# Performance work log

Hardware: AMD Instinct MI355X
Metric: run time of the kernel (lower is better)

## Reference

```python
import jax, jax.numpy as jnp
import numpy as np

B, D, C = 32, 30, 4        # batch, input spatial, in-channels
KS = 3                     # kernel size per dim
OD = D - KS + 1            # 28 (valid padding, stride 1)
P = OD ** 3                # 21952 output positions
K = (KS ** 3) * C          # 108 taps per output position
F = 4                      # output filters


def _patches(x):
    # x: [B, D, D, D, C] -> [B, P, K]
    xt = jnp.transpose(x, (0, 4, 1, 2, 3))  # NCDHW
    p = jax.lax.conv_general_dilated_patches(
        xt, filter_shape=(KS, KS, KS), window_strides=(1, 1, 1), padding='VALID')
    # p: [B, C*KS^3, OD, OD, OD]
    p = jnp.transpose(p, (0, 2, 3, 4, 1))
    return p.reshape(p.shape[0], P, K)


def _local_conv(x, W):
    # Locally-connected 3D conv (unshared weights) == structured sparse matmul.
    # W: [P, K, F] one weight per (output position, tap, filter).
    return jnp.einsum('bpk,pkf->bpf', _patches(x), W)


def setup_inputs() -> dict:
    key = jax.random.key(0)
    ks = jax.random.split(key, 7)
    x = jax.random.normal(ks[0], (B, D, D, D, C), jnp.float32)
    kernel_loc = jax.random.normal(ks[1], (P, K, F), jnp.float32) * 0.05
    kernel_rho = jax.random.normal(ks[2], (P, K, F), jnp.float32) * 0.1 - 5.0  # softplus -> small scale
    bias = jax.random.normal(ks[3], (F,), jnp.float32) * 0.05
    eps = jax.random.normal(ks[4], (P, K, F), jnp.float32)
    sign_in = jax.random.rademacher(ks[5], (B, D, D, D, C), jnp.float32)
    sign_out = jax.random.rademacher(ks[6], (B, P, F), jnp.float32)
    return dict(x=x, kernel_loc=kernel_loc, kernel_rho=kernel_rho, bias=bias,
                eps=eps, sign_in=sign_in, sign_out=sign_out)


def reference(x, kernel_loc, kernel_rho, bias, eps, sign_in, sign_out):
    # Flipout estimator: deterministic mean path + sign-perturbed noise path.
    scale = jax.nn.softplus(kernel_rho)
    out = _local_conv(x, kernel_loc)                                  # [B, P, F]
    out = out + sign_out * _local_conv(x * sign_in, scale * eps)      # flipout perturbation
    out = out + bias                                                  # per-filter bias (channels_last)
    return out.reshape(x.shape[0], OD, OD, OD, F)
```

## Files before the change

kernel.cpp:

```cpp
#include <hip/hip_runtime.h>


constexpr int Bn   = 32;
constexpr int Dn   = 30;
constexpr int Cn   = 4;
constexpr int ODn  = 28;
constexpr int Pn   = ODn * ODn * ODn;
constexpr int Tt   = 27;
constexpr int Kn   = Tt * Cn;
constexpr int PPB  = 16;
constexpr int NT   = Pn / PPB;
constexpr int THREADS = 512;
constexpr int WSTRIDE = Kn + 1;
constexpr int GRID = NT;

__device__ __forceinline__ unsigned bf16rne(float f) {
    unsigned u = __float_as_uint(f);
    return (u + 0x7fffu + ((u >> 16) & 1u)) >> 16;
}
__device__ __forceinline__ float bflo(unsigned u) { return __uint_as_float(u << 16); }
__device__ __forceinline__ float bfhi(unsigned u) { return __uint_as_float(u & 0xffff0000u); }

__device__ __forceinline__ uint4 pack_w(const float4 L, const float4 R, const float4 E) {
    float nx = (R.x > 15.f ? R.x : __logf(1.f + __expf(R.x))) * E.x;
    float ny = (R.y > 15.f ? R.y : __logf(1.f + __expf(R.y))) * E.y;
    float nz = (R.z > 15.f ? R.z : __logf(1.f + __expf(R.z))) * E.z;
    float nw = (R.w > 15.f ? R.w : __logf(1.f + __expf(R.w))) * E.w;
    uint4 pk;
    pk.x = bf16rne(L.x) | (bf16rne(L.y) << 16);
    pk.y = bf16rne(L.z) | (bf16rne(L.w) << 16);
    pk.z = bf16rne(nx)  | (bf16rne(ny) << 16);
    pk.w = bf16rne(nz)  | (bf16rne(nw) << 16);
    return pk;
}

__global__ __launch_bounds__(THREADS) void lc3d_flipout_kernel(
    const float* __restrict__ x,
    const float* __restrict__ loc,
    const float* __restrict__ rho,
    const float* __restrict__ bias,
    const float* __restrict__ eps,
    const float* __restrict__ sgn_in,
    const float* __restrict__ sgn_out,
    float* __restrict__ out)
{
    __shared__ uint4 wsh[PPB * WSTRIDE];

    const int tid = threadIdx.x;

    const int xcd  = blockIdx.x & 7;
    const int slot = blockIdx.x >> 3;
    const int Tx = (xcd < 4) ? xcd * 172 : 688 + (xcd - 4) * 171;
    const int p_base = (Tx + slot) * PPB;

    {
        const float4* loc4 = (const float4*)loc + (size_t)p_base * Kn;
        const float4* rho4 = (const float4*)rho + (size_t)p_base * Kn;
        const float4* eps4 = (const float4*)eps + (size_t)p_base * Kn;
        const int g0 = tid, g1 = tid + 512, g2 = tid + 1024;
        const float4 L0 = loc4[g0], R0 = rho4[g0], E0 = eps4[g0];
        const float4 L1 = loc4[g1], R1 = rho4[g1], E1 = eps4[g1];
        const float4 L2 = loc4[g2], R2 = rho4[g2], E2 = eps4[g2];
        {
            const int plc = g0 / Kn, k = g0 - plc * Kn;
            wsh[plc * WSTRIDE + k] = pack_w(L0, R0, E0);
        }
        {
            const int plc = g1 / Kn, k = g1 - plc * Kn;
            wsh[plc * WSTRIDE + k] = pack_w(L1, R1, E1);
        }
        {
            const int plc = g2 / Kn, k = g2 - plc * Kn;
            wsh[plc * WSTRIDE + k] = pack_w(L2, R2, E2);
        }
        if (tid < PPB * Kn - 1536) {
            const int g3 = tid + 1536;
            const int plc = g3 / Kn, k = g3 - plc * Kn;
            wsh[plc * WSTRIDE + k] = pack_w(loc4[g3], rho4[g3], eps4[g3]);
        }
    }
    __syncthreads();

    const int pl = tid & 15;
    const int b  = tid >> 4;
    const int p  = p_base + pl;
    const int od = p / (ODn * ODn);
    const int prem = p - od * (ODn * ODn);
    const int oh = prem / ODn;
    const int ow = prem - oh * ODn;
    const float4* x4 = (const float4*)x;
    const float4* s4 = (const float4*)sgn_in;
    const size_t v0 = (((size_t)b * Dn + od) * Dn + oh) * Dn + ow;
    const uint4* wp = wsh + pl * WSTRIDE;

    float a0=0.f,a1=0.f,a2=0.f,a3=0.f, n0=0.f,n1=0.f,n2=0.f,n3=0.f;

#define CHAN(c, x_c, s_c)                                                    \
    {                                                                        \
        const uint4 wv = wp[(c) * Tt + t];                                   \
        const float m0 = bflo(wv.x), m1 = bfhi(wv.x);                        \
        const float m2 = bflo(wv.y), m3 = bfhi(wv.y);                        \
        const float q0 = bflo(wv.z), q1 = bfhi(wv.z);                        \
        const float q2 = bflo(wv.w), q3 = bfhi(wv.w);                        \
        a0 = fmaf(x_c, m0, a0); a1 = fmaf(x_c, m1, a1);                      \
        a2 = fmaf(x_c, m2, a2); a3 = fmaf(x_c, m3, a3);                      \
        const float ya = (x_c) * (s_c);                                      \
        n0 = fmaf(ya, q0, n0); n1 = fmaf(ya, q1, n1);                        \
        n2 = fmaf(ya, q2, n2); n3 = fmaf(ya, q3, n3);                        \
    }

    #pragma unroll
    for (int kd = 0; kd < 3; ++kd) {
        #pragma unroll
        for (int kh = 0; kh < 3; ++kh) {
            const int roff = (kd * Dn + kh) * Dn;
            #pragma unroll
            for (int kw = 0; kw < 3; ++kw) {
                const int t = (kd * 3 + kh) * 3 + kw;
                const float4 xa = x4[v0 + roff + kw];
                const float4 sa = s4[v0 + roff + kw];
                CHAN(0, xa.x, sa.x);
                CHAN(1, xa.y, sa.y);
                CHAN(2, xa.z, sa.z);
                CHAN(3, xa.w, sa.w);
            }
        }
    }
#undef CHAN

    const float4 bi = *(const float4*)bias;
    const size_t ob = (size_t)b * Pn + p;
    const float4 so = ((const float4*)sgn_out)[ob];
    float4 o;
    o.x = fmaf(so.x, n0, a0) + bi.x;
    o.y = fmaf(so.y, n1, a1) + bi.y;
    o.z = fmaf(so.z, n2, a2) + bi.z;
    o.w = fmaf(so.w, n3, a3) + bi.w;
    ((float4*)out)[ob] = o;
}

extern "C" void kernel_launch(void* const* d_in, const int* in_sizes, int n_in,
                              void* d_out, int out_size, void* d_ws, size_t ws_size,
                              hipStream_t stream) {
    const float* x    = (const float*)d_in[0];
    const float* loc  = (const float*)d_in[1];
    const float* rho  = (const float*)d_in[2];
    const float* bias = (const float*)d_in[3];
    const float* eps  = (const float*)d_in[4];
    const float* si   = (const float*)d_in[5];
    const float* so   = (const float*)d_in[6];
    float* out = (float*)d_out;

    lc3d_flipout_kernel<<<dim3(GRID), dim3(THREADS), 0, stream>>>(
        x, loc, rho, bias, eps, si, so, out);
}
```

Before: 206.1 us.

## Make kernel persistent with double-buffered weight prefetch interleaved with compute

```diff
diff --git a/kernel.cpp b/kernel.cpp
--- a/kernel.cpp
+++ b/kernel.cpp
@@ -8,11 +8,14 @@
 constexpr int Pn   = ODn * ODn * ODn;
 constexpr int Tt   = 27;
 constexpr int Kn   = Tt * Cn;
-constexpr int PPB  = 16;
+constexpr int PPB  = 8;
 constexpr int NT   = Pn / PPB;
-constexpr int THREADS = 512;
+constexpr int THREADS = 256;
 constexpr int WSTRIDE = Kn + 1;
-constexpr int GRID = NT;
+constexpr int UNITS = PPB * Kn;
+constexpr int TPX  = NT / 8;
+constexpr int SLOTS = 128;
+constexpr int GRID = SLOTS * 8;
 
 __device__ __forceinline__ unsigned bf16rne(float f) {
     unsigned u = __float_as_uint(f);
@@ -44,56 +47,46 @@
     const float* __restrict__ sgn_out,
     float* __restrict__ out)
 {
-    __shared__ uint4 wsh[PPB * WSTRIDE];
+    __shared__ uint4 wsh[2][PPB * WSTRIDE];
 
     const int tid = threadIdx.x;
 
     const int xcd  = blockIdx.x & 7;
     const int slot = blockIdx.x >> 3;
-    const int Tx = (xcd < 4) ? xcd * 172 : 688 + (xcd - 4) * 171;
-    const int p_base = (Tx + slot) * PPB;
+    const int tA = (slot * TPX) >> 7;
+    const int tB = ((slot + 1) * TPX) >> 7;
+    const int T0 = xcd * TPX + tA;
+    const int n  = tB - tA;
+
+    const float4* loc4 = (const float4*)loc;
+    const float4* rho4 = (const float4*)rho;
+    const float4* eps4 = (const float4*)eps;
+    const float4* x4   = (const float4*)x;
+    const float4* s4   = (const float4*)sgn_in;
+    const float4  bi   = *(const float4*)bias;
+
+    const int pl = tid & 7;
+    const int b  = tid >> 3;
+    const bool tail = (tid < UNITS - 3 * THREADS);
+
+    const int g0 = tid, g1 = tid + 256, g2 = tid + 512, g3 = tid + 768;
+    const int o0 = (g0 / Kn) * WSTRIDE + (g0 % Kn);
+    const int o1 = (g1 / Kn) * WSTRIDE + (g1 % Kn);
+    const int o2 = (g2 / Kn) * WSTRIDE + (g2 % Kn);
+    const int o3 = (g3 / Kn) * WSTRIDE + (g3 % Kn);
 
     {
-        const float4* loc4 = (const float4*)loc + (size_t)p_base * Kn;
-        const float4* rho4 = (const float4*)rho + (size_t)p_base * Kn;
-        const float4* eps4 = (const float4*)eps + (size_t)p_base * Kn;
-        const int g0 = tid, g1 = tid + 512, g2 = tid + 1024;
-        const float4 L0 = loc4[g0], R0 = rho4[g0], E0 = eps4[g0];
-        const float4 L1 = loc4[g1], R1 = rho4[g1], E1 = eps4[g1];
-        const float4 L2 = loc4[g2], R2 = rho4[g2], E2 = eps4[g2];
-        {
-            const int plc = g0 / Kn, k = g0 - plc * Kn;
-            wsh[plc * WSTRIDE + k] = pack_w(L0, R0, E0);
-        }
-        {
-            const int plc = g1 / Kn, k = g1 - plc * Kn;
-            wsh[plc * WSTRIDE + k] = pack_w(L1, R1, E1);
-        }
-        {
-            const int plc = g2 / Kn, k = g2 - plc * Kn;
-            wsh[plc * WSTRIDE + k] = pack_w(L2, R2, E2);
-        }
-        if (tid < PPB * Kn - 1536) {
-            const int g3 = tid + 1536;
-            const int plc = g3 / Kn, k = g3 - plc * Kn;
-            wsh[plc * WSTRIDE + k] = pack_w(loc4[g3], rho4[g3], eps4[g3]);
-        }
+        const size_t base = (size_t)T0 * UNITS;
+        const float4 L0 = loc4[base + g0], R0 = rho4[base + g0], E0 = eps4[base + g0];
+        const float4 L1 = loc4[base + g1], R1 = rho4[base + g1], E1 = eps4[base + g1];
+        const float4 L2 = loc4[base + g2], R2 = rho4[base + g2], E2 = eps4[base + g2];
+        wsh[0][o0] = pack_w(L0, R0, E0);
+        wsh[0][o1] = pack_w(L1, R1, E1);
+        wsh[0][o2] = pack_w(L2, R2, E2);
+        if (tail)
+            wsh[0][o3] = pack_w(loc4[base + g3], rho4[base + g3], eps4[base + g3]);
     }
     __syncthreads();
-
-    const int pl = tid & 15;
-    const int b  = tid >> 4;
-    const int p  = p_base + pl;
-    const int od = p / (ODn * ODn);
-    const int prem = p - od * (ODn * ODn);
-    const int oh = prem / ODn;
-    const int ow = prem - oh * ODn;
-    const float4* x4 = (const float4*)x;
-    const float4* s4 = (const float4*)sgn_in;
-    const size_t v0 = (((size_t)b * Dn + od) * Dn + oh) * Dn + ow;
-    const uint4* wp = wsh + pl * WSTRIDE;
-
-    float a0=0.f,a1=0.f,a2=0.f,a3=0.f, n0=0.f,n1=0.f,n2=0.f,n3=0.f;
 
 #define CHAN(c, x_c, s_c)                                                    \
     {                                                                        \
@@ -109,34 +102,73 @@
         n2 = fmaf(ya, q2, n2); n3 = fmaf(ya, q3, n3);                        \
     }
 
-    #pragma unroll
-    for (int kd = 0; kd < 3; ++kd) {
-        #pragma unroll
-        for (int kh = 0; kh < 3; ++kh) {
-            const int roff = (kd * Dn + kh) * Dn;
-            #pragma unroll
-            for (int kw = 0; kw < 3; ++kw) {
-                const int t = (kd * 3 + kh) * 3 + kw;
-                const float4 xa = x4[v0 + roff + kw];
-                const float4 sa = s4[v0 + roff + kw];
-                CHAN(0, xa.x, sa.x);
-                CHAN(1, xa.y, sa.y);
-                CHAN(2, xa.z, sa.z);
-                CHAN(3, xa.w, sa.w);
-            }
+#define CHUNK(t_lo, t_hi)                                                    \
+    _Pragma("unroll")                                                        \
+    for (int t = (t_lo); t < (t_hi); ++t) {                                  \
+        const int kd = t / 9, kh = (t % 9) / 3, kw = t % 3;                  \
+        const int off = (kd * Dn + kh) * Dn + kw;                            \
+        const float4 xa = x4[v0 + off];                                      \
+        const float4 sa = s4[v0 + off];                                      \
+        CHAN(0, xa.x, sa.x);                                                 \
+        CHAN(1, xa.y, sa.y);                                                 \
+        CHAN(2, xa.z, sa.z);                                                 \
+        CHAN(3, xa.w, sa.w);                                                 \
+    }
+
+#pragma unroll 1
+    for (int i = 0; i < n; ++i) {
+        const int cur = i & 1;
+        const int T = T0 + i;
+        const int p = T * PPB + pl;
+        const int od = p / (ODn * ODn);
+        const int prem = p - od * (ODn * ODn);
+        const int oh = prem / ODn;
+        const int ow = prem - oh * ODn;
+        const size_t v0 = (((size_t)b * Dn + od) * Dn + oh) * Dn + ow;
+        const uint4* wp = &wsh[cur][pl * WSTRIDE];
+        const bool pf = (i + 1 < n);
+        const size_t nb = (size_t)(T + 1) * UNITS;
+
+        float a0=0.f,a1=0.f,a2=0.f,a3=0.f, n0=0.f,n1=0.f,n2=0.f,n3=0.f;
+
+        float4 PL0, PR0, PE0, PL1, PR1, PE1, PL2, PR2, PE2, PL3, PR3, PE3;
+        if (pf) { PL0 = loc4[nb + g0]; PR0 = rho4[nb + g0]; PE0 = eps4[nb + g0]; }
+
+        CHUNK(0, 9)
+
+        if (pf) {
+            wsh[cur ^ 1][o0] = pack_w(PL0, PR0, PE0);
+            PL1 = loc4[nb + g1]; PR1 = rho4[nb + g1]; PE1 = eps4[nb + g1];
+            if (tail) { PL3 = loc4[nb + g3]; PR3 = rho4[nb + g3]; PE3 = eps4[nb + g3]; }
         }
+
+        CHUNK(9, 18)
+
+        if (pf) {
+            wsh[cur ^ 1][o1] = pack_w(PL1, PR1, PE1);
+            PL2 = loc4[nb + g2]; PR2 = rho4[nb + g2]; PE2 = eps4[nb + g2];
+        }
+
+        CHUNK(18, 27)
+
+        if (pf) {
+            wsh[cur ^ 1][o2] = pack_w(PL2, PR2, PE2);
+            if (tail) wsh[cur ^ 1][o3] = pack_w(PL3, PR3, PE3);
+        }
+
+        const size_t ob = (size_t)b * Pn + p;
+        const float4 so = ((const float4*)sgn_out)[ob];
+        float4 o;
+        o.x = fmaf(so.x, n0, a0) + bi.x;
+        o.y = fmaf(so.y, n1, a1) + bi.y;
+        o.z = fmaf(so.z, n2, a2) + bi.z;
+        o.w = fmaf(so.w, n3, a3) + bi.w;
+        ((float4*)out)[ob] = o;
+
+        __syncthreads();
     }
+#undef CHUNK
 #undef CHAN
-
-    const float4 bi = *(const float4*)bias;
-    const size_t ob = (size_t)b * Pn + p;
-    const float4 so = ((const float4*)sgn_out)[ob];
-    float4 o;
-    o.x = fmaf(so.x, n0, a0) + bi.x;
-    o.y = fmaf(so.y, n1, a1) + bi.y;
-    o.z = fmaf(so.z, n2, a2) + bi.z;
-    o.w = fmaf(so.w, n3, a3) + bi.w;
-    ((float4*)out)[ob] = o;
 }
 
 extern "C" void kernel_launch(void* const* d_in, const int* in_sizes, int n_in,
```

After: 534.8 us. 159% more time.

## Prepack noise weights to bf16 workspace and stream tiles via async LDS double-buffering

Applied to the files above, without the earlier changes.

```diff
diff --git a/kernel.cpp b/kernel.cpp
--- a/kernel.cpp
+++ b/kernel.cpp
@@ -8,11 +8,22 @@
 constexpr int Pn   = ODn * ODn * ODn;
 constexpr int Tt   = 27;
 constexpr int Kn   = Tt * Cn;
-constexpr int PPB  = 16;
+constexpr int PPB  = 8;
 constexpr int NT   = Pn / PPB;
-constexpr int THREADS = 512;
-constexpr int WSTRIDE = Kn + 1;
-constexpr int GRID = NT;
+constexpr int TPX  = NT / 8;
+
+constexpr int THREADS_B = 256;
+constexpr int SLOTS  = 96;
+constexpr int GRID_B = SLOTS * 8;
+constexpr int LOC_UNITS   = PPB * Kn;
+constexpr int NOISE_UNITS = PPB * Kn / 2;
+constexpr int TILE_UNITS  = LOC_UNITS + NOISE_UNITS;
+constexpr int NCHUNK = 21;
+constexpr int BUF_UNITS = NCHUNK * 64;
+constexpr int NOISE_BYTES_PER_TILE = PPB * Kn * 8;
+constexpr int LOC_BYTES_PER_TILE   = PPB * Kn * 16;
+
+constexpr size_t WS_NEEDED = (size_t)Pn * Kn * 8;
 
 __device__ __forceinline__ unsigned bf16rne(float f) {
     unsigned u = __float_as_uint(f);
@@ -20,6 +31,175 @@
 }
 __device__ __forceinline__ float bflo(unsigned u) { return __uint_as_float(u << 16); }
 __device__ __forceinline__ float bfhi(unsigned u) { return __uint_as_float(u & 0xffff0000u); }
+
+typedef const __attribute__((address_space(1))) void GASV;
+typedef __attribute__((address_space(3))) void LASV;
+__device__ __forceinline__ void gld_lds16(const void* g, void* l) {
+    __builtin_amdgcn_global_load_lds((GASV*)g, (LASV*)l, 16, 0, 0);
+}
+
+__global__ __launch_bounds__(256) void pack_noise_kernel(
+    const float* __restrict__ rho, const float* __restrict__ eps,
+    uint2* __restrict__ ws)
+{
+    const long NU = (long)Pn * Kn;
+    const float4* r4 = (const float4*)rho;
+    const float4* e4 = (const float4*)eps;
+    for (long g = (long)blockIdx.x * 256 + threadIdx.x; g < NU;
+         g += (long)gridDim.x * 256) {
+        const float4 R = r4[g];
+        const float4 E = e4[g];
+        const float nx = (R.x > 15.f ? R.x : __logf(1.f + __expf(R.x))) * E.x;
+        const float ny = (R.y > 15.f ? R.y : __logf(1.f + __expf(R.y))) * E.y;
+        const float nz = (R.z > 15.f ? R.z : __logf(1.f + __expf(R.z))) * E.z;
+        const float nw = (R.w > 15.f ? R.w : __logf(1.f + __expf(R.w))) * E.w;
+        uint2 o;
+        o.x = bf16rne(nx) | (bf16rne(ny) << 16);
+        o.y = bf16rne(nz) | (bf16rne(nw) << 16);
+        ws[g] = o;
+    }
+}
+
+__global__ __launch_bounds__(THREADS_B) void lc3d_flipout_dma(
+    const float* __restrict__ x,
+    const float* __restrict__ loc,
+    const float* __restrict__ bias,
+    const uint2* __restrict__ ws,
+    const float* __restrict__ sgn_in,
+    const float* __restrict__ sgn_out,
+    float* __restrict__ out)
+{
+    __shared__ uint4 wsh[2][BUF_UNITS];
+
+    const int tid = threadIdx.x;
+    const int wv = tid >> 6, ln = tid & 63;
+
+    const int xcd  = blockIdx.x & 7;
+    const int slot = blockIdx.x >> 3;
+    const int tA = (slot * TPX) / SLOTS;
+    const int tB = ((slot + 1) * TPX) / SLOTS;
+    const int T0 = xcd * TPX + tA;
+    const int n  = tB - tA;
+
+    const int nch = (wv == 0) ? 6 : 5;
+    const int cb  = (wv == 0) ? 0 : (1 + 5 * wv);
+    int  coff[6];
+    bool cws[6];
+    int  cchk[6];
+    #pragma unroll
+    for (int j = 0; j < 6; ++j) {
+        int ch = (j < nch) ? (cb + j) : cb;
+        const int u = ch * 64 + ln;
+        if (u < LOC_UNITS) {
+            const int k = u >> 3, pp = u & 7;
+            coff[j] = pp * (Kn * 16) + k * 16;
+            cws[j] = false;
+        } else if (u < TILE_UNITS) {
+            coff[j] = (u - LOC_UNITS) * 16;
+            cws[j] = true;
+        } else {
+            coff[j] = 0; cws[j] = false;
+        }
+        cchk[j] = ch;
+    }
+
+#define ISSUE(TT, BI)                                                        \
+    {                                                                        \
+        const char* bl = (const char*)loc + (size_t)(TT) * LOC_BYTES_PER_TILE;   \
+        const char* bw = (const char*)ws  + (size_t)(TT) * NOISE_BYTES_PER_TILE; \
+        char* lb = (char*)&wsh[BI][0];                                       \
+        _Pragma("unroll")                                                    \
+        for (int j = 0; j < 6; ++j)                                          \
+            if (j < nch)                                                     \
+                gld_lds16((cws[j] ? bw : bl) + coff[j], lb + cchk[j] * 1024); \
+    }
+
+    ISSUE(T0, 0)
+    asm volatile("s_waitcnt vmcnt(0)" ::: "memory");
+    __syncthreads();
+
+    const float4* x4 = (const float4*)x;
+    const float4* s4 = (const float4*)sgn_in;
+    const float4  bi = *(const float4*)bias;
+    const int pl = tid & 7;
+    const int b  = tid >> 3;
+
+    float4 o_prev;
+    size_t ob_prev = 0;
+    bool have_prev = false;
+
+#define CHAN(c, x_c, s_c)                                                    \
+    {                                                                        \
+        const int kk = (c) * Tt + t;                                         \
+        const float4 m = *(const float4*)&lc4[kk * 8 + pl];                  \
+        const uint2 nz = nz2[pl * Kn + kk];                                  \
+        a0 = fmaf(x_c, m.x, a0); a1 = fmaf(x_c, m.y, a1);                    \
+        a2 = fmaf(x_c, m.z, a2); a3 = fmaf(x_c, m.w, a3);                    \
+        const float ya = (x_c) * (s_c);                                      \
+        n0 = fmaf(ya, bflo(nz.x), n0); n1 = fmaf(ya, bfhi(nz.x), n1);        \
+        n2 = fmaf(ya, bflo(nz.y), n2); n3 = fmaf(ya, bfhi(nz.y), n3);        \
+    }
+
+#pragma unroll 1
+    for (int i = 0; i < n; ++i) {
+        const int bufi = i & 1;
+        const int T = T0 + i;
+
+        if (i + 1 < n) ISSUE(T + 1, bufi ^ 1)
+
+        const int p  = T * PPB + pl;
+        const int od = p / (ODn * ODn);
+        const int prem = p - od * (ODn * ODn);
+        const int oh = prem / ODn;
+        const int ow = prem - oh * ODn;
+        const size_t v0 = (((size_t)b * Dn + od) * Dn + oh) * Dn + ow;
+        const size_t ob = (size_t)b * Pn + p;
+        const float4 so = ((const float4*)sgn_out)[ob];
+
+        const uint4* lc4 = &wsh[bufi][0];
+        const uint2* nz2 = (const uint2*)&wsh[bufi][LOC_UNITS];
+
+        float a0=0.f,a1=0.f,a2=0.f,a3=0.f, n0=0.f,n1=0.f,n2=0.f,n3=0.f;
+
+        #pragma unroll
+        for (int kd = 0; kd < 3; ++kd) {
+            #pragma unroll
+            for (int kh = 0; kh < 3; ++kh) {
+                const int roff = (kd * Dn + kh) * Dn;
+                #pragma unroll
+                for (int kw = 0; kw < 3; ++kw) {
+                    const int t = (kd * 3 + kh) * 3 + kw;
+                    const float4 xa = x4[v0 + roff + kw];
+                    const float4 sa = s4[v0 + roff + kw];
+                    CHAN(0, xa.x, sa.x);
+                    CHAN(1, xa.y, sa.y);
+                    CHAN(2, xa.z, sa.z);
+                    CHAN(3, xa.w, sa.w);
+                }
+            }
+        }
+
+        float4 o;
+        o.x = fmaf(so.x, n0, a0) + bi.x;
+        o.y = fmaf(so.y, n1, a1) + bi.y;
+        o.z = fmaf(so.z, n2, a2) + bi.z;
+        o.w = fmaf(so.w, n3, a3) + bi.w;
+
+        asm volatile("s_waitcnt vmcnt(0)" ::: "memory");
+        __syncthreads();
+
+        if (have_prev) ((float4*)out)[ob_prev] = o_prev;
+        ((float4*)out)[ob] = o;
+        have_prev = false;
+        (void)o_prev; (void)ob_prev;
+    }
+#undef CHAN
+#undef ISSUE
+}
+
+constexpr int PPB_F = 16;
+constexpr int NT_F  = Pn / PPB_F;
+constexpr int WSTRIDE_F = Kn + 1;
 
 __device__ __forceinline__ uint4 pack_w(const float4 L, const float4 R, const float4 E) {
     float nx = (R.x > 15.f ? R.x : __logf(1.f + __expf(R.x))) * E.x;
@@ -34,25 +214,18 @@
     return pk;
 }
 
-__global__ __launch_bounds__(THREADS) void lc3d_flipout_kernel(
-    const float* __restrict__ x,
-    const float* __restrict__ loc,
-    const float* __restrict__ rho,
-    const float* __restrict__ bias,
-    const float* __restrict__ eps,
-    const float* __restrict__ sgn_in,
-    const float* __restrict__ sgn_out,
-    float* __restrict__ out)
+__global__ __launch_bounds__(512) void lc3d_fallback(
+    const float* __restrict__ x, const float* __restrict__ loc,
+    const float* __restrict__ rho, const float* __restrict__ bias,
+    const float* __restrict__ eps, const float* __restrict__ sgn_in,
+    const float* __restrict__ sgn_out, float* __restrict__ out)
 {
-    __shared__ uint4 wsh[PPB * WSTRIDE];
-
+    __shared__ uint4 wsh[PPB_F * WSTRIDE_F];
     const int tid = threadIdx.x;
-
     const int xcd  = blockIdx.x & 7;
     const int slot = blockIdx.x >> 3;
     const int Tx = (xcd < 4) ? xcd * 172 : 688 + (xcd - 4) * 171;
-    const int p_base = (Tx + slot) * PPB;
-
+    const int p_base = (Tx + slot) * PPB_F;
     {
         const float4* loc4 = (const float4*)loc + (size_t)p_base * Kn;
         const float4* rho4 = (const float4*)rho + (size_t)p_base * Kn;
@@ -61,26 +234,16 @@
         const float4 L0 = loc4[g0], R0 = rho4[g0], E0 = eps4[g0];
         const float4 L1 = loc4[g1], R1 = rho4[g1], E1 = eps4[g1];
         const float4 L2 = loc4[g2], R2 = rho4[g2], E2 = eps4[g2];
-        {
-            const int plc = g0 / Kn, k = g0 - plc * Kn;
-            wsh[plc * WSTRIDE + k] = pack_w(L0, R0, E0);
-        }
-        {
-            const int plc = g1 / Kn, k = g1 - plc * Kn;
-            wsh[plc * WSTRIDE + k] = pack_w(L1, R1, E1);
-        }
-        {
-            const int plc = g2 / Kn, k = g2 - plc * Kn;
-            wsh[plc * WSTRIDE + k] = pack_w(L2, R2, E2);
-        }
-        if (tid < PPB * Kn - 1536) {
+        { const int plc = g0 / Kn, k = g0 - plc * Kn; wsh[plc * WSTRIDE_F + k] = pack_w(L0, R0, E0); }
+        { const int plc = g1 / Kn, k = g1 - plc * Kn; wsh[plc * WSTRIDE_F + k] = pack_w(L1, R1, E1); }
+        { const int plc = g2 / Kn, k = g2 - plc * Kn; wsh[plc * WSTRIDE_F + k] = pack_w(L2, R2, E2); }
+        if (tid < PPB_F * Kn - 1536) {
             const int g3 = tid + 1536;
             const int plc = g3 / Kn, k = g3 - plc * Kn;
-            wsh[plc * WSTRIDE + k] = pack_w(loc4[g3], rho4[g3], eps4[g3]);
+            wsh[plc * WSTRIDE_F + k] = pack_w(loc4[g3], rho4[g3], eps4[g3]);
         }
     }
     __syncthreads();
-
     const int pl = tid & 15;
     const int b  = tid >> 4;
     const int p  = p_base + pl;
@@ -91,26 +254,19 @@
     const float4* x4 = (const float4*)x;
     const float4* s4 = (const float4*)sgn_in;
     const size_t v0 = (((size_t)b * Dn + od) * Dn + oh) * Dn + ow;
-    const uint4* wp = wsh + pl * WSTRIDE;
-
+    const uint4* wp = wsh + pl * WSTRIDE_F;
     float a0=0.f,a1=0.f,a2=0.f,a3=0.f, n0=0.f,n1=0.f,n2=0.f,n3=0.f;
-
-#define CHAN(c, x_c, s_c)                                                    \
+#define CHANF(c, x_c, s_c)                                                   \
     {                                                                        \
-        const uint4 wv = wp[(c) * Tt + t];                                   \
-        const float m0 = bflo(wv.x), m1 = bfhi(wv.x);                        \
-        const float m2 = bflo(wv.y), m3 = bfhi(wv.y);                        \
-        const float q0 = bflo(wv.z), q1 = bfhi(wv.z);                        \
-        const float q2 = bflo(wv.w), q3 = bfhi(wv.w);                        \
-        a0 = fmaf(x_c, m0, a0); a1 = fmaf(x_c, m1, a1);                      \
-        a2 = fmaf(x_c, m2, a2); a3 = fmaf(x_c, m3, a3);                      \
+        const uint4 wvv = wp[(c) * Tt + t];                                  \
+        a0 = fmaf(x_c, bflo(wvv.x), a0); a1 = fmaf(x_c, bfhi(wvv.x), a1);    \
+        a2 = fmaf(x_c, bflo(wvv.y), a2); a3 = fmaf(x_c, bfhi(wvv.y), a3);    \
         const float ya = (x_c) * (s_c);                                      \
-        n0 = fmaf(ya, q0, n0); n1 = fmaf(ya, q1, n1);                        \
-        n2 = fmaf(ya, q2, n2); n3 = fmaf(ya, q3, n3);                        \
-    }
-
+        n0 = fmaf(ya, bflo(wvv.z), n0); n1 = fmaf(ya, bfhi(wvv.z), n1);      \
+        n2 = fmaf(ya, bflo(wvv.w), n2); n3 = fmaf(ya, bfhi(wvv.w), n3);      \
+    }
     #pragma unroll
-    for (int kd = 0; kd < 3; ++kd) {
+    for (int kd = 0; kd < 3; ++kd)
         #pragma unroll
         for (int kh = 0; kh < 3; ++kh) {
             const int roff = (kd * Dn + kh) * Dn;
@@ -119,15 +275,11 @@
                 const int t = (kd * 3 + kh) * 3 + kw;
                 const float4 xa = x4[v0 + roff + kw];
                 const float4 sa = s4[v0 + roff + kw];
-                CHAN(0, xa.x, sa.x);
-                CHAN(1, xa.y, sa.y);
-                CHAN(2, xa.z, sa.z);
-                CHAN(3, xa.w, sa.w);
+                CHANF(0, xa.x, sa.x); CHANF(1, xa.y, sa.y);
+                CHANF(2, xa.z, sa.z); CHANF(3, xa.w, sa.w);
             }
         }
-    }
-#undef CHAN
-
+#undef CHANF
     const float4 bi = *(const float4*)bias;
     const size_t ob = (size_t)b * Pn + p;
     const float4 so = ((const float4*)sgn_out)[ob];
@@ -151,6 +303,13 @@
     const float* so   = (const float*)d_in[6];
     float* out = (float*)d_out;
 
-    lc3d_flipout_kernel<<<dim3(GRID), dim3(THREADS), 0, stream>>>(
-        x, loc, rho, bias, eps, si, so, out);
-}
+    if (d_ws != nullptr && ws_size >= WS_NEEDED) {
+        pack_noise_kernel<<<dim3(2048), dim3(256), 0, stream>>>(
+            rho, eps, (uint2*)d_ws);
+        lc3d_flipout_dma<<<dim3(GRID_B), dim3(THREADS_B), 0, stream>>>(
+            x, loc, bias, (const uint2*)d_ws, si, so, out);
+    } else {
+        lc3d_fallback<<<dim3(NT_F), dim3(512), 0, stream>>>(
+            x, loc, rho, bias, eps, si, so, out);
+    }
+}
```

New measurement: 223.9 us. +8.6%, slower.

## Halve positions per block and split taps across two thread halves

Applied to the files above, without the earlier changes.

```diff
diff --git a/kernel.cpp b/kernel.cpp
--- a/kernel.cpp
+++ b/kernel.cpp
@@ -8,11 +8,13 @@
 constexpr int Pn   = ODn * ODn * ODn;
 constexpr int Tt   = 27;
 constexpr int Kn   = Tt * Cn;
-constexpr int PPB  = 16;
+constexpr int PPB  = 8;
 constexpr int NT   = Pn / PPB;
+constexpr int TPX  = NT / 8;
 constexpr int THREADS = 512;
 constexpr int WSTRIDE = Kn + 1;
 constexpr int GRID = NT;
+constexpr int STAGE_UNITS = PPB * Kn;
 
 __device__ __forceinline__ unsigned bf16rne(float f) {
     unsigned u = __float_as_uint(f);
@@ -50,39 +52,29 @@
 
     const int xcd  = blockIdx.x & 7;
     const int slot = blockIdx.x >> 3;
-    const int Tx = (xcd < 4) ? xcd * 172 : 688 + (xcd - 4) * 171;
-    const int p_base = (Tx + slot) * PPB;
+    const int p_base = (xcd * TPX + slot) * PPB;
 
     {
         const float4* loc4 = (const float4*)loc + (size_t)p_base * Kn;
         const float4* rho4 = (const float4*)rho + (size_t)p_base * Kn;
         const float4* eps4 = (const float4*)eps + (size_t)p_base * Kn;
-        const int g0 = tid, g1 = tid + 512, g2 = tid + 1024;
+        const bool two = tid < (STAGE_UNITS - THREADS);
+        const int g0 = tid;
+        const int g1 = two ? tid + THREADS : tid;
         const float4 L0 = loc4[g0], R0 = rho4[g0], E0 = eps4[g0];
         const float4 L1 = loc4[g1], R1 = rho4[g1], E1 = eps4[g1];
-        const float4 L2 = loc4[g2], R2 = rho4[g2], E2 = eps4[g2];
-        {
-            const int plc = g0 / Kn, k = g0 - plc * Kn;
-            wsh[plc * WSTRIDE + k] = pack_w(L0, R0, E0);
-        }
-        {
-            const int plc = g1 / Kn, k = g1 - plc * Kn;
-            wsh[plc * WSTRIDE + k] = pack_w(L1, R1, E1);
-        }
-        {
-            const int plc = g2 / Kn, k = g2 - plc * Kn;
-            wsh[plc * WSTRIDE + k] = pack_w(L2, R2, E2);
-        }
-        if (tid < PPB * Kn - 1536) {
-            const int g3 = tid + 1536;
-            const int plc = g3 / Kn, k = g3 - plc * Kn;
-            wsh[plc * WSTRIDE + k] = pack_w(loc4[g3], rho4[g3], eps4[g3]);
+        { const int p_ = g0 / Kn, k_ = g0 - p_ * Kn;
+          wsh[p_ * WSTRIDE + k_] = pack_w(L0, R0, E0); }
+        if (two) {
+            const int p_ = g1 / Kn, k_ = g1 - p_ * Kn;
+            wsh[p_ * WSTRIDE + k_] = pack_w(L1, R1, E1);
         }
     }
     __syncthreads();
 
-    const int pl = tid & 15;
-    const int b  = tid >> 4;
+    const int pl = tid & 7;
+    const int b  = (tid >> 3) & 31;
+    const int kh = tid >> 8;
     const int p  = p_base + pl;
     const int od = p / (ODn * ODn);
     const int prem = p - od * (ODn * ODn);
@@ -95,48 +87,60 @@
 
     float a0=0.f,a1=0.f,a2=0.f,a3=0.f, n0=0.f,n1=0.f,n2=0.f,n3=0.f;
 
-#define CHAN(c, x_c, s_c)                                                    \
+#define CHAN(c, t, x_c, s_c)                                                 \
     {                                                                        \
-        const uint4 wv = wp[(c) * Tt + t];                                   \
-        const float m0 = bflo(wv.x), m1 = bfhi(wv.x);                        \
-        const float m2 = bflo(wv.y), m3 = bfhi(wv.y);                        \
-        const float q0 = bflo(wv.z), q1 = bfhi(wv.z);                        \
-        const float q2 = bflo(wv.w), q3 = bfhi(wv.w);                        \
-        a0 = fmaf(x_c, m0, a0); a1 = fmaf(x_c, m1, a1);                      \
-        a2 = fmaf(x_c, m2, a2); a3 = fmaf(x_c, m3, a3);                      \
+        const uint4 wv = wp[(c) * Tt + (t)];                                 \
+        a0 = fmaf(x_c, bflo(wv.x), a0); a1 = fmaf(x_c, bfhi(wv.x), a1);      \
+        a2 = fmaf(x_c, bflo(wv.y), a2); a3 = fmaf(x_c, bfhi(wv.y), a3);      \
         const float ya = (x_c) * (s_c);                                      \
-        n0 = fmaf(ya, q0, n0); n1 = fmaf(ya, q1, n1);                        \
-        n2 = fmaf(ya, q2, n2); n3 = fmaf(ya, q3, n3);                        \
+        n0 = fmaf(ya, bflo(wv.z), n0); n1 = fmaf(ya, bfhi(wv.z), n1);        \
+        n2 = fmaf(ya, bflo(wv.w), n2); n3 = fmaf(ya, bfhi(wv.w), n3);        \
     }
 
-    #pragma unroll
-    for (int kd = 0; kd < 3; ++kd) {
-        #pragma unroll
-        for (int kh = 0; kh < 3; ++kh) {
-            const int roff = (kd * Dn + kh) * Dn;
-            #pragma unroll
-            for (int kw = 0; kw < 3; ++kw) {
-                const int t = (kd * 3 + kh) * 3 + kw;
-                const float4 xa = x4[v0 + roff + kw];
-                const float4 sa = s4[v0 + roff + kw];
-                CHAN(0, xa.x, sa.x);
-                CHAN(1, xa.y, sa.y);
-                CHAN(2, xa.z, sa.z);
-                CHAN(3, xa.w, sa.w);
-            }
-        }
+#define TAP(t)                                                               \
+    {                                                                        \
+        constexpr int kd_ = (t) / 9, kh_ = ((t) % 9) / 3, kw_ = (t) % 3;     \
+        const float4 xa = x4[v0 + (kd_ * Dn + kh_) * Dn + kw_];              \
+        const float4 sa = s4[v0 + (kd_ * Dn + kh_) * Dn + kw_];              \
+        CHAN(0, t, xa.x, sa.x)                                               \
+        CHAN(1, t, xa.y, sa.y)                                               \
+        CHAN(2, t, xa.z, sa.z)                                               \
+        CHAN(3, t, xa.w, sa.w)                                               \
     }
+
+    if (kh == 0) {
+        TAP(0)  TAP(1)  TAP(2)  TAP(3)  TAP(4)  TAP(5)  TAP(6)
+        TAP(7)  TAP(8)  TAP(9)  TAP(10) TAP(11) TAP(12) TAP(13)
+    } else {
+        TAP(14) TAP(15) TAP(16) TAP(17) TAP(18) TAP(19) TAP(20)
+        TAP(21) TAP(22) TAP(23) TAP(24) TAP(25) TAP(26)
+    }
+#undef TAP
 #undef CHAN
 
-    const float4 bi = *(const float4*)bias;
-    const size_t ob = (size_t)b * Pn + p;
-    const float4 so = ((const float4*)sgn_out)[ob];
-    float4 o;
-    o.x = fmaf(so.x, n0, a0) + bi.x;
-    o.y = fmaf(so.y, n1, a1) + bi.y;
-    o.z = fmaf(so.z, n2, a2) + bi.z;
-    o.w = fmaf(so.w, n3, a3) + bi.w;
-    ((float4*)out)[ob] = o;
+    __syncthreads();
+    float4* sc = (float4*)wsh;
+    if (kh == 1) {
+        sc[tid - 256]       = make_float4(a0, a1, a2, a3);
+        sc[256 + tid - 256] = make_float4(n0, n1, n2, n3);
+    }
+    __syncthreads();
+    if (kh == 0) {
+        const float4 pa = sc[tid];
+        const float4 pn = sc[256 + tid];
+        a0 += pa.x; a1 += pa.y; a2 += pa.z; a3 += pa.w;
+        n0 += pn.x; n1 += pn.y; n2 += pn.z; n3 += pn.w;
+
+        const float4 bi = *(const float4*)bias;
+        const size_t ob = (size_t)b * Pn + p;
+        const float4 so = ((const float4*)sgn_out)[ob];
+        float4 o;
+        o.x = fmaf(so.x, n0, a0) + bi.x;
+        o.y = fmaf(so.y, n1, a1) + bi.y;
+        o.z = fmaf(so.z, n2, a2) + bi.z;
+        o.w = fmaf(so.w, n3, a3) + bi.w;
+        ((float4*)out)[ob] = o;
+    }
 }
 
 extern "C" void kernel_launch(void* const* d_in, const int* in_sizes, int n_in,
```

Result: slower. 236.1 us (+14.6%).
